# Optimization experiments

Measured on AMD Instinct MI355X. Metric: run time of the kernel, lower is better.

## Reference

```python
import jax, jax.numpy as jnp
import numpy as np

B, S, H = 4, 1024, 2560          # batch, seq, hidden_size
E, K, F = 32, 6, 1536            # num_experts, top_k, moe_intermediate_size
SHARED_F = 2 * 1536              # moe_num_shared_experts * moe_intermediate_size
NORM_MIN = 1e-12                 # config.moe_norm_min


def setup_inputs() -> dict:
    key = jax.random.key(0)
    ks = jax.random.split(key, 9)
    rnd = lambda k, shape, scale=0.02: jax.random.normal(k, shape, dtype=jnp.float32) * scale
    return {
        "hidden_states": jax.random.normal(ks[0], (B, S, H), dtype=jnp.float32),
        "router_w": rnd(ks[1], (E, H)),              # Ernie4_5_MoeTopKRouter.weight (fp32)
        "router_bias": jnp.zeros((E,), jnp.float32),  # moe_statics.e_score_correction_bias
        "gate_w": rnd(ks[2], (E, H, F)),
        "up_w": rnd(ks[3], (E, H, F)),
        "down_w": rnd(ks[4], (E, F, H)),
        "shared_gate_w": rnd(ks[5], (H, SHARED_F)),
        "shared_up_w": rnd(ks[6], (H, SHARED_F)),
        "shared_down_w": rnd(ks[7], (SHARED_F, H)),
    }


def _mlp(x, gw, uw, dw):
    # Ernie4_5_MoeMLP: down( silu(gate(x)) * up(x) ), no biases
    return (jax.nn.silu(x @ gw) * (x @ uw)) @ dw


def _forward(hidden_states, router_w, router_bias, gate_w, up_w, down_w,
             shared_gate_w, shared_up_w, shared_down_w):
    T = B * S
    xt = hidden_states.reshape(T, H)

    # shared experts path (always-on dense MLP)
    shared_out = _mlp(xt, shared_gate_w, shared_up_w, shared_down_w)

    # router: fp32 linear -> softmax -> (+ correction bias) -> top-k -> renorm
    logits = xt.astype(jnp.float32) @ router_w.T            # [T, E]
    probs = jax.nn.softmax(logits, axis=-1)
    top_w, top_i = jax.lax.top_k(probs + router_bias[None, :], K)  # [T, K]
    top_w = top_w / jnp.clip(jnp.sum(top_w, axis=-1, keepdims=True), NORM_MIN)
    top_w = top_w.astype(hidden_states.dtype)

    # expert combine: loop over the fixed expert set; per-token combine weight
    # cw[t] = sum_k top_w[t,k] * (top_i[t,k] == e)  (matches one-hot dispatch +
    # index_add_ scatter combine of the original)
    out = jnp.zeros_like(xt)
    for e in range(E):
        cw = jnp.sum(jnp.where(top_i == e, top_w, 0.0), axis=-1)  # [T]
        y = _mlp(xt, gate_w[e], up_w[e], down_w[e])               # [T, H]
        out = out + cw[:, None] * y

    out = out + shared_out
    return out.reshape(B, S, H)


def reference(hidden_states, router_w, router_bias, gate_w, up_w, down_w,
              shared_gate_w, shared_up_w, shared_down_w):
    return _forward(hidden_states, router_w, router_bias, gate_w, up_w, down_w,
                    shared_gate_w, shared_up_w, shared_down_w)
```

## Files before the change

kernel.cpp:

```cpp
#include <hip/hip_runtime.h>
#include <hip/hip_bf16.h>
#include <math.h>

#define T_TOK 4096
#define HID   2560
#define NEXP  32
#define KTOP  6
#define FF    1536
#define SFF   3072
#define MAXP  (T_TOK*KTOP)

typedef __attribute__((ext_vector_type(8))) short short8;
typedef __attribute__((ext_vector_type(4))) float f32x4;

static __device__ __forceinline__ unsigned short f2bf(float x){
  return __builtin_bit_cast(unsigned short, (__bf16)x);
}
static __device__ __forceinline__ float bf2f(unsigned short u){
  unsigned int x = ((unsigned int)u) << 16;
  return __builtin_bit_cast(float, x);
}

static __device__ __forceinline__ void gload_lds16(const void* g, void* l){
  __builtin_amdgcn_global_load_lds(
      (const __attribute__((address_space(1))) unsigned int*)g,
      (__attribute__((address_space(3))) unsigned int*)l, 16, 0, 0);
}

__global__ void k_cast_x(const float* __restrict__ x, unsigned short* __restrict__ xb){
  int i = (blockIdx.x * 256 + threadIdx.x) * 4;
  float4 v = *(const float4*)(x + i);
  ushort4 o;
  o.x = f2bf(v.x); o.y = f2bf(v.y); o.z = f2bf(v.z); o.w = f2bf(v.w);
  *(ushort4*)(xb + i) = o;
}

__global__ __launch_bounds__(256)
void k_transpose(const float* __restrict__ in, unsigned short* __restrict__ out,
                 const int R, const int C, const long long outBS){
  const size_t bi = (size_t)blockIdx.z * (size_t)R * C;
  const size_t bo = (size_t)blockIdx.z * (size_t)outBS;
  __shared__ unsigned short t2[64][72];
  const int r0 = blockIdx.y * 64, c0 = blockIdx.x * 64;
  const int tid = threadIdx.x;
  const int cr = tid & 15;
  const int rr = tid >> 4;
#pragma unroll
  for (int i = 0; i < 4; ++i){
    const int r = rr + 16*i;
    float4 v = *(const float4*)(in + bi + (size_t)(r0 + r)*C + c0 + cr*4);
    ushort4 p;
    p.x = f2bf(v.x); p.y = f2bf(v.y); p.z = f2bf(v.z); p.w = f2bf(v.w);
    *(ushort4*)(&t2[r][cr*4]) = p;
  }
  __syncthreads();
  const int rw = tid & 7;
  const int ro = tid >> 3;
#pragma unroll
  for (int i = 0; i < 2; ++i){
    const int c = ro + 32*i;
    ushort4 a, b;
    a.x = t2[rw*8+0][c]; a.y = t2[rw*8+1][c]; a.z = t2[rw*8+2][c]; a.w = t2[rw*8+3][c];
    b.x = t2[rw*8+4][c]; b.y = t2[rw*8+5][c]; b.z = t2[rw*8+6][c]; b.w = t2[rw*8+7][c];
    unsigned short* op = out + bo + (size_t)(c0 + c)*R + r0 + rw*8;
    *(ushort4*)(op)     = a;
    *(ushort4*)(op + 4) = b;
  }
}

__global__ void k_router(const float* __restrict__ x, const float* __restrict__ rw,
                         const float* __restrict__ rb, float* __restrict__ top_w,
                         int* __restrict__ top_i, int* __restrict__ counts){
  const int lane = threadIdx.x & 63;
  const int wv   = threadIdx.x >> 6;
  const int t    = blockIdx.x * 4 + wv;
  const float* xr = x + (size_t)t * HID;
  float xv[40];
#pragma unroll
  for (int i = 0; i < 40; ++i) xv[i] = xr[lane + 64*i];
  float sc[32];
  for (int e = 0; e < 32; ++e){
    const float* w = rw + (size_t)e * HID;
    float s = 0.f;
#pragma unroll
    for (int i = 0; i < 40; ++i) s = fmaf(xv[i], w[lane + 64*i], s);
#pragma unroll
    for (int o = 32; o; o >>= 1) s += __shfl_xor(s, o);
    sc[e] = s;
  }
  float mx = sc[0];
#pragma unroll
  for (int e = 1; e < 32; ++e) mx = fmaxf(mx, sc[e]);
  float se = 0.f;
#pragma unroll
  for (int e = 0; e < 32; ++e){ sc[e] = expf(sc[e] - mx); se += sc[e]; }
  const float inv = 1.f / se;
#pragma unroll
  for (int e = 0; e < 32; ++e) sc[e] = sc[e] * inv + rb[e];

  unsigned chosen = 0; float swv[KTOP]; int sid[KTOP]; float wsum = 0.f;
#pragma unroll
  for (int k = 0; k < KTOP; ++k){
    float bv = -1e30f; int bi = 0;
#pragma unroll
    for (int e = 0; e < 32; ++e){
      bool ok = !((chosen >> e) & 1u);
      if (ok && sc[e] > bv){ bv = sc[e]; bi = e; }
    }
    chosen |= 1u << bi; swv[k] = bv; sid[k] = bi; wsum += bv;
  }
  const float dn = fmaxf(wsum, 1e-12f);
  if (lane < KTOP){
    top_w[t*KTOP + lane] = swv[lane] / dn;
    top_i[t*KTOP + lane] = sid[lane];
    atomicAdd(counts + sid[lane], 1);
  }
}

__global__ void k_scan(const int* __restrict__ counts, int* __restrict__ offsets){
  if (threadIdx.x == 0){
    int a = 0;
    for (int e = 0; e < NEXP; ++e){ offsets[e] = a; a += counts[e]; }
    offsets[NEXP] = a;
  }
}

__global__ void k_scatter(const int* __restrict__ top_i, const float* __restrict__ top_w,
                          const int* __restrict__ offsets, int* __restrict__ cursor,
                          int* __restrict__ pair_tok, float* __restrict__ pair_w){
  const int t = blockIdx.x * 256 + threadIdx.x;
  if (t >= T_TOK) return;
#pragma unroll
  for (int k = 0; k < KTOP; ++k){
    int e = top_i[t*KTOP + k];
    int pos = offsets[e] + atomicAdd(cursor + e, 1);
    pair_tok[pos] = t;
    pair_w[pos]   = top_w[t*KTOP + k];
  }
}

template<int F8>
__global__ __launch_bounds__(256)
void k_swiglu(const unsigned short* __restrict__ y, unsigned short* __restrict__ act){
  const int i = blockIdx.x * 256 + threadIdx.x;
  const int p = i / F8, c = i % F8;
  const unsigned short* row = y + (size_t)p * (2*F8*8);
  short8 g8 = *(const short8*)(row + c*8);
  short8 u8 = *(const short8*)(row + F8*8 + c*8);
  short8 o;
#pragma unroll
  for (int j = 0; j < 8; ++j){
    float g = bf2f((unsigned short)g8[j]);
    float u = bf2f((unsigned short)u8[j]);
    float s = (g / (1.f + expf(-g))) * u;
    o[j] = (short)f2bf(s);
  }
  *(short8*)(act + (size_t)p*F8*8 + c*8) = o;
}

template<bool GROUPED, bool GATHER, int OUT>
__global__ __launch_bounds__(512, 2)
void k_gemm(const unsigned short* __restrict__ A,
            const unsigned short* __restrict__ BT,
            void* __restrict__ outp,
            const int* __restrict__ pair_tok, const float* __restrict__ pair_w,
            const int* __restrict__ counts, const int* __restrict__ offsets,
            const int N, const int K, const int ntiles)
{
  const int NH = K >> 5;
  const int total = gridDim.x;
  const int phys  = blockIdx.x;
  const int logical = (phys & 7) * (total >> 3) + (phys >> 3);
  const int mt   = logical & 15;
  const int rest = logical >> 4;
  const int n0 = (rest % ntiles) << 8;
  const int e  = rest / ntiles;

  int M, base;
  if (GROUPED){ M = counts[e]; base = offsets[e]; }
  else        { M = T_TOK;     base = 0; }
  if (mt * 256 >= M) return;
  const unsigned short* Bb = BT + (size_t)e * (size_t)N * K;

  __shared__ unsigned short AS[4*8192];
  __shared__ unsigned short BS[4*8192];

  const int tid  = threadIdx.x;
  const int lane = tid & 63;
  const int w    = tid >> 6;
  const int wr = w >> 2, wc = w & 3;

  const int lrow = lane >> 2, lchunk = lane & 3;
  const int swz = (lchunk ^ ((lrow >> 1) & 3)) * 8;
  const unsigned short *ap0, *ap1, *bp0, *bp1;
  {
    const int r0 = w*32 + lrow, r1 = w*32 + 16 + lrow;
    int i0 = min(mt*256 + r0, M - 1);
    int i1 = min(mt*256 + r1, M - 1);
    int rowA0 = GATHER ? pair_tok[base + i0] : (GROUPED ? base + i0 : i0);
    int rowA1 = GATHER ? pair_tok[base + i1] : (GROUPED ? base + i1 : i1);
    ap0 = A + (size_t)rowA0 * K + swz;
    ap1 = A + (size_t)rowA1 * K + swz;
    bp0 = Bb + (size_t)(n0 + r0) * K + swz;
    bp1 = Bb + (size_t)(n0 + r1) * K + swz;
  }

  const f32x4 zero = {0.f,0.f,0.f,0.f};
  f32x4 acc[8][4];
#pragma unroll
  for (int m = 0; m < 8; ++m)
#pragma unroll
    for (int n = 0; n < 4; ++n) acc[m][n] = zero;

  const int fr = lane & 15;
  const int fg = ((lane >> 4) ^ ((lane >> 1) & 3)) * 16;

#define STAGE(h)                                                            \
  { const int _s = (h) & 3; const size_t _k = (size_t)(h) * 32;             \
    gload_lds16(ap0 + _k, (char*)AS + _s*16384 + (w*32)*64);                \
    gload_lds16(ap1 + _k, (char*)AS + _s*16384 + (w*32+16)*64);             \
    gload_lds16(bp0 + _k, (char*)BS + _s*16384 + (w*32)*64);                \
    gload_lds16(bp1 + _k, (char*)BS + _s*16384 + (w*32+16)*64); }

  STAGE(0) STAGE(1) STAGE(2)
  asm volatile("s_waitcnt vmcnt(8)" ::: "memory");
  __builtin_amdgcn_s_barrier();

#pragma unroll 4
  for (int h = 0; h < NH; ++h){
    const int s = h & 3;
    const char* _as = (const char*)AS + s*16384;
    const char* _bs = (const char*)BS + s*16384;
    short8 bq[4], af[8];
#pragma unroll
    for (int n = 0; n < 4; ++n)
      bq[n] = *(const short8*)(_bs + (wc*64 + n*16 + fr)*64 + fg);
#pragma unroll
    for (int m = 0; m < 8; ++m)
      af[m] = *(const short8*)(_as + (wr*128 + m*16 + fr)*64 + fg);
    if (h + 3 < NH) STAGE(h + 3)
    __builtin_amdgcn_s_setprio(1);
#pragma unroll
    for (int m = 0; m < 8; ++m)
#pragma unroll
      for (int n = 0; n < 4; ++n)
        acc[m][n] = __builtin_amdgcn_mfma_f32_16x16x32_bf16(af[m], bq[n], acc[m][n], 0, 0, 0);
    __builtin_amdgcn_s_setprio(0);
    if (h + 3 < NH)      asm volatile("s_waitcnt vmcnt(8)" ::: "memory");
    else if (h + 2 < NH) asm volatile("s_waitcnt vmcnt(4)" ::: "memory");
    else if (h + 1 < NH) asm volatile("s_waitcnt vmcnt(0)" ::: "memory");
    __builtin_amdgcn_s_barrier();
  }
#undef STAGE

#pragma unroll
  for (int m = 0; m < 8; ++m)
#pragma unroll
    for (int j = 0; j < 4; ++j){
      const int rr = mt*256 + wr*128 + m*16 + (lane >> 4)*4 + j;
      if (rr < M){
        const int col = n0 + wc*64 + (lane & 15);
        if (OUT == 0){
          unsigned short* orow = (unsigned short*)outp + (size_t)(base + rr) * N + col;
#pragma unroll
          for (int n = 0; n < 4; ++n) orow[n*16] = f2bf(acc[m][n][j]);
        } else if (OUT == 1){
          const int p = base + rr;
          const int tok = pair_tok[p];
          const float pw = pair_w[p];
          float* orow = (float*)outp + (size_t)tok * HID + col;
#pragma unroll
          for (int n = 0; n < 4; ++n) atomicAdd(orow + n*16, acc[m][n][j] * pw);
        } else {
          float* orow = (float*)outp + (size_t)rr * N + col;
#pragma unroll
          for (int n = 0; n < 4; ++n) orow[n*16] = acc[m][n][j];
        }
      }
    }
}

extern "C" void kernel_launch(void* const* d_in, const int* in_sizes, int n_in,
                              void* d_out, int out_size, void* d_ws, size_t ws_size,
                              hipStream_t stream)
{
  (void)in_sizes; (void)n_in; (void)out_size; (void)ws_size;
  const float* hid = (const float*)d_in[0];
  const float* rw  = (const float*)d_in[1];
  const float* rb  = (const float*)d_in[2];
  const float* gw  = (const float*)d_in[3];
  const float* uw  = (const float*)d_in[4];
  const float* dw  = (const float*)d_in[5];
  const float* sgw = (const float*)d_in[6];
  const float* suw = (const float*)d_in[7];
  const float* sdw = (const float*)d_in[8];
  float* out = (float*)d_out;

  char* ws = (char*)d_ws;
  size_t o = 0;
  unsigned short* xb   = (unsigned short*)(ws + o); o += (size_t)T_TOK*HID*2;
  unsigned short* act  = (unsigned short*)(ws + o); o += (size_t)MAXP*FF*2;
  unsigned short* sact = (unsigned short*)(ws + o); o += (size_t)T_TOK*SFF*2;
  unsigned short* y    = (unsigned short*)(ws + o); o += (size_t)MAXP*2*FF*2;
  unsigned short* sy   = (unsigned short*)(ws + o); o += (size_t)T_TOK*2*SFF*2;
  unsigned short* Wbuf = (unsigned short*)(ws + o);
  unsigned short* guT  = Wbuf;
  unsigned short* sguT = Wbuf + (size_t)NEXP*2*FF*HID;
  unsigned short* dT   = Wbuf;
  unsigned short* sdT  = Wbuf + (size_t)NEXP*HID*FF;
  o += (size_t)NEXP*2*FF*HID*2 + (size_t)2*SFF*HID*2;
  float* top_w    = (float*)(ws + o); o += (size_t)T_TOK*KTOP*4;
  int*   top_i    = (int*)(ws + o);   o += (size_t)T_TOK*KTOP*4;
  float* pair_w   = (float*)(ws + o); o += (size_t)MAXP*4;
  int*   pair_tok = (int*)(ws + o);   o += (size_t)MAXP*4;
  int*   counts   = (int*)(ws + o);   o += NEXP*4;
  int*   offsets  = (int*)(ws + o);   o += (NEXP+1)*4;
  int*   cursor   = (int*)(ws + o);   o += NEXP*4;

  hipMemsetAsync(counts, 0, (NEXP + (NEXP+1) + NEXP) * sizeof(int), stream);

  k_cast_x<<<(T_TOK*HID)/1024, 256, 0, stream>>>(hid, xb);
  k_router<<<T_TOK/4, 256, 0, stream>>>(hid, rw, rb, top_w, top_i, counts);
  k_scan<<<1, 64, 0, stream>>>(counts, offsets);
  k_scatter<<<T_TOK/256, 256, 0, stream>>>(top_i, top_w, offsets, cursor, pair_tok, pair_w);

  k_transpose<<<dim3(FF/64,  HID/64, NEXP), 256, 0, stream>>>(gw,  guT,                    HID, FF,  (long long)2*FF*HID);
  k_transpose<<<dim3(FF/64,  HID/64, NEXP), 256, 0, stream>>>(uw,  guT + (size_t)FF*HID,   HID, FF,  (long long)2*FF*HID);
  k_transpose<<<dim3(SFF/64, HID/64, 1),    256, 0, stream>>>(sgw, sguT,                   HID, SFF, 0);
  k_transpose<<<dim3(SFF/64, HID/64, 1),    256, 0, stream>>>(suw, sguT + (size_t)SFF*HID, HID, SFF, 0);

  k_gemm<true,  true,  0><<<16*(2*FF/256)*NEXP, 512, 0, stream>>>(
      xb, guT, y, pair_tok, nullptr, counts, offsets, 2*FF, HID, 2*FF/256);
  k_gemm<false, false, 0><<<16*(2*SFF/256), 512, 0, stream>>>(
      xb, sguT, sy, nullptr, nullptr, nullptr, nullptr, 2*SFF, HID, 2*SFF/256);
  k_swiglu<FF/8><<<(MAXP*(FF/8))/256, 256, 0, stream>>>(y, act);
  k_swiglu<SFF/8><<<(T_TOK*(SFF/8))/256, 256, 0, stream>>>(sy, sact);

  k_transpose<<<dim3(HID/64, FF/64,  NEXP), 256, 0, stream>>>(dw,  dT,  FF,  HID, (long long)HID*FF);
  k_transpose<<<dim3(HID/64, SFF/64, 1),    256, 0, stream>>>(sdw, sdT, SFF, HID, 0);

  k_gemm<false, false, 2><<<16*(HID/256), 512, 0, stream>>>(
      sact, sdT, out, nullptr, nullptr, nullptr, nullptr, HID, SFF, HID/256);
  k_gemm<true,  false, 1><<<16*(HID/256)*NEXP, 512, 0, stream>>>(
      act, dT, out, pair_tok, pair_w, counts, offsets, HID, FF, HID/256);
}
```

Measured before the change: 1.792 ms.

## Fuse SwiGLU into gate/up GEMM epilogue and merge expert/shared launches

Replaces the separate gate/up GEMMs and SwiGLU kernels with one kernel that computes gate and up accumulators side by side over 128-wide column tiles and applies silu(g)*u in the epilogue, writing bf16 activations directly. Expert and shared tiles are merged into a single grid. This removes the large intermediate y/sy round-trip through memory and several launches. Both GEMM loops now prefetch LDS fragments for the next step after the MFMAs, behind a sched_barrier, and use a shallower vmcnt wait. The cost is a narrower N tile with two accumulator sets, which changes register pressure and A-tile reuse per block.

```diff
diff --git a/kernel.cpp b/kernel.cpp
--- a/kernel.cpp
+++ b/kernel.cpp
@@ -15,10 +15,6 @@
 
 static __device__ __forceinline__ unsigned short f2bf(float x){
   return __builtin_bit_cast(unsigned short, (__bf16)x);
-}
-static __device__ __forceinline__ float bf2f(unsigned short u){
-  unsigned int x = ((unsigned int)u) << 16;
-  return __builtin_bit_cast(float, x);
 }
 
 static __device__ __forceinline__ void gload_lds16(const void* g, void* l){
@@ -139,34 +135,148 @@
   }
 }
 
-template<int F8>
-__global__ __launch_bounds__(256)
-void k_swiglu(const unsigned short* __restrict__ y, unsigned short* __restrict__ act){
-  const int i = blockIdx.x * 256 + threadIdx.x;
-  const int p = i / F8, c = i % F8;
-  const unsigned short* row = y + (size_t)p * (2*F8*8);
-  short8 g8 = *(const short8*)(row + c*8);
-  short8 u8 = *(const short8*)(row + F8*8 + c*8);
-  short8 o;
-#pragma unroll
-  for (int j = 0; j < 8; ++j){
-    float g = bf2f((unsigned short)g8[j]);
-    float u = bf2f((unsigned short)u8[j]);
-    float s = (g / (1.f + expf(-g))) * u;
-    o[j] = (short)f2bf(s);
-  }
-  *(short8*)(act + (size_t)p*F8*8 + c*8) = o;
-}
-
-template<bool GROUPED, bool GATHER, int OUT>
 __global__ __launch_bounds__(512, 2)
-void k_gemm(const unsigned short* __restrict__ A,
-            const unsigned short* __restrict__ BT,
-            void* __restrict__ outp,
+void k_gufused(const unsigned short* __restrict__ A,
+               const unsigned short* __restrict__ gT, const unsigned short* __restrict__ uT,
+               const unsigned short* __restrict__ sgT, const unsigned short* __restrict__ suT,
+               unsigned short* __restrict__ act, unsigned short* __restrict__ sact,
+               const int* __restrict__ pair_tok,
+               const int* __restrict__ counts, const int* __restrict__ offsets)
+{
+  constexpr int K = HID;
+  constexpr int NH = K >> 5;
+  constexpr int EXPTILES = NEXP * (FF/128);
+  const int total = gridDim.x;
+  const int phys  = blockIdx.x;
+  const int logical = (phys & 7) * (total >> 3) + (phys >> 3);
+  const int mt   = logical & 15;
+  const int rest = logical >> 4;
+
+  int M, base, n0, N; bool gather;
+  const unsigned short *Bg, *Bu; unsigned short* op;
+  if (rest < EXPTILES){
+    const int e = rest / (FF/128);
+    n0 = (rest % (FF/128)) * 128;
+    M = counts[e]; base = offsets[e]; gather = true;
+    Bg = gT + (size_t)e * FF * HID; Bu = uT + (size_t)e * FF * HID;
+    op = act; N = FF;
+  } else {
+    const int s = rest - EXPTILES;
+    n0 = s * 128; M = T_TOK; base = 0; gather = false;
+    Bg = sgT; Bu = suT; op = sact; N = SFF;
+  }
+  if (mt * 256 >= M) return;
+
+  __shared__ unsigned short AS[4*8192];
+  __shared__ unsigned short BgS[4*4096];
+  __shared__ unsigned short BuS[4*4096];
+
+  const int tid  = threadIdx.x;
+  const int lane = tid & 63;
+  const int w    = tid >> 6;
+  const int wr = w >> 1, wc = w & 1;
+
+  const int lrow = lane >> 2, lchunk = lane & 3;
+  const int swz = (lchunk ^ ((lrow >> 1) & 3)) * 8;
+  const unsigned short *ap0, *ap1, *bgp, *bup;
+  {
+    const int r0 = w*32 + lrow, r1 = w*32 + 16 + lrow;
+    int i0 = min(mt*256 + r0, M - 1);
+    int i1 = min(mt*256 + r1, M - 1);
+    int rowA0 = gather ? pair_tok[base + i0] : i0;
+    int rowA1 = gather ? pair_tok[base + i1] : i1;
+    ap0 = A + (size_t)rowA0 * K + swz;
+    ap1 = A + (size_t)rowA1 * K + swz;
+    const int rb = w*16 + lrow;
+    const int swzb = (lchunk ^ ((rb >> 1) & 3)) * 8;
+    bgp = Bg + (size_t)(n0 + rb) * K + swzb;
+    bup = Bu + (size_t)(n0 + rb) * K + swzb;
+  }
+
+  const f32x4 zero = {0.f,0.f,0.f,0.f};
+  f32x4 accg[4][4], accu[4][4];
+#pragma unroll
+  for (int m = 0; m < 4; ++m)
+#pragma unroll
+    for (int n = 0; n < 4; ++n){ accg[m][n] = zero; accu[m][n] = zero; }
+
+  const int fr = lane & 15;
+  const int fg = ((lane >> 4) ^ ((lane >> 1) & 3)) * 16;
+  short8 af[4], bg[4], bu[4];
+
+#define GU_STAGE(h)                                                         \
+  { const int _s = (h) & 3; const size_t _k = (size_t)(h) * 32;             \
+    gload_lds16(ap0 + _k, (char*)AS  + _s*16384 + (w*32)*64);               \
+    gload_lds16(ap1 + _k, (char*)AS  + _s*16384 + (w*32+16)*64);            \
+    gload_lds16(bgp + _k, (char*)BgS + _s*8192  + (w*16)*64);               \
+    gload_lds16(bup + _k, (char*)BuS + _s*8192  + (w*16)*64); }
+
+#define GU_RFRAGS(h)                                                        \
+  { const int _s = (h) & 3;                                                 \
+    const char* _as = (const char*)AS  + _s*16384;                          \
+    const char* _bg = (const char*)BgS + _s*8192;                           \
+    const char* _bu = (const char*)BuS + _s*8192;                           \
+    _Pragma("unroll")                                                       \
+    for (int m = 0; m < 4; ++m)                                             \
+      af[m] = *(const short8*)(_as + (wr*64 + m*16 + fr)*64 + fg);          \
+    _Pragma("unroll")                                                       \
+    for (int n = 0; n < 4; ++n){                                            \
+      bg[n] = *(const short8*)(_bg + (wc*64 + n*16 + fr)*64 + fg);          \
+      bu[n] = *(const short8*)(_bu + (wc*64 + n*16 + fr)*64 + fg); } }
+
+  GU_STAGE(0) GU_STAGE(1) GU_STAGE(2)
+  asm volatile("s_waitcnt vmcnt(4)" ::: "memory");
+  __builtin_amdgcn_s_barrier();
+  GU_RFRAGS(0)
+
+#pragma unroll 4
+  for (int h = 0; h < NH; ++h){
+    __builtin_amdgcn_s_setprio(1);
+#pragma unroll
+    for (int m = 0; m < 4; ++m)
+#pragma unroll
+      for (int n = 0; n < 4; ++n){
+        accg[m][n] = __builtin_amdgcn_mfma_f32_16x16x32_bf16(af[m], bg[n], accg[m][n], 0, 0, 0);
+        accu[m][n] = __builtin_amdgcn_mfma_f32_16x16x32_bf16(af[m], bu[n], accu[m][n], 0, 0, 0);
+      }
+    __builtin_amdgcn_s_setprio(0);
+    __builtin_amdgcn_sched_barrier(0);
+    if (h + 3 < NH) GU_STAGE(h + 3)
+    if (h + 1 < NH) GU_RFRAGS(h + 1)
+    if (h + 3 < NH) asm volatile("s_waitcnt vmcnt(4)" ::: "memory");
+    else            asm volatile("s_waitcnt vmcnt(0)" ::: "memory");
+    __builtin_amdgcn_s_barrier();
+  }
+#undef GU_STAGE
+#undef GU_RFRAGS
+
+#pragma unroll
+  for (int m = 0; m < 4; ++m)
+#pragma unroll
+    for (int j = 0; j < 4; ++j){
+      const int rr = mt*256 + wr*64 + m*16 + (lane >> 4)*4 + j;
+      if (rr < M){
+        unsigned short* orow = op + (size_t)(base + rr) * N + n0 + wc*64 + fr;
+#pragma unroll
+        for (int n = 0; n < 4; ++n){
+          float g = accg[m][n][j], u = accu[m][n][j];
+          float s = (g / (1.f + expf(-g))) * u;
+          orow[n*16] = f2bf(s);
+        }
+      }
+    }
+}
+
+template<bool GROUPED, int OUT>
+__global__ __launch_bounds__(512, 2)
+void k_down(const unsigned short* __restrict__ Aact,
+            const unsigned short* __restrict__ BT, float* __restrict__ outp,
             const int* __restrict__ pair_tok, const float* __restrict__ pair_w,
             const int* __restrict__ counts, const int* __restrict__ offsets,
-            const int N, const int K, const int ntiles)
+            const int K)
 {
+  constexpr int N = HID;
+  constexpr int ntiles = N >> 8;
   const int NH = K >> 5;
   const int total = gridDim.x;
   const int phys  = blockIdx.x;
@@ -197,10 +307,8 @@
     const int r0 = w*32 + lrow, r1 = w*32 + 16 + lrow;
     int i0 = min(mt*256 + r0, M - 1);
     int i1 = min(mt*256 + r1, M - 1);
-    int rowA0 = GATHER ? pair_tok[base + i0] : (GROUPED ? base + i0 : i0);
-    int rowA1 = GATHER ? pair_tok[base + i1] : (GROUPED ? base + i1 : i1);
-    ap0 = A + (size_t)rowA0 * K + swz;
-    ap1 = A + (size_t)rowA1 * K + swz;
+    ap0 = Aact + (size_t)(base + i0) * K + swz;
+    ap1 = Aact + (size_t)(base + i1) * K + swz;
     bp0 = Bb + (size_t)(n0 + r0) * K + swz;
     bp1 = Bb + (size_t)(n0 + r1) * K + swz;
   }
@@ -214,31 +322,33 @@
 
   const int fr = lane & 15;
   const int fg = ((lane >> 4) ^ ((lane >> 1) & 3)) * 16;
-
-#define STAGE(h)                                                            \
+  short8 af[8], bq[4];
+
+#define DN_STAGE(h)                                                         \
   { const int _s = (h) & 3; const size_t _k = (size_t)(h) * 32;             \
     gload_lds16(ap0 + _k, (char*)AS + _s*16384 + (w*32)*64);                \
     gload_lds16(ap1 + _k, (char*)AS + _s*16384 + (w*32+16)*64);             \
     gload_lds16(bp0 + _k, (char*)BS + _s*16384 + (w*32)*64);                \
     gload_lds16(bp1 + _k, (char*)BS + _s*16384 + (w*32+16)*64); }
 
-  STAGE(0) STAGE(1) STAGE(2)
-  asm volatile("s_waitcnt vmcnt(8)" ::: "memory");
+#define DN_RFRAGS(h)                                                        \
+  { const int _s = (h) & 3;                                                 \
+    const char* _as = (const char*)AS + _s*16384;                           \
+    const char* _bs = (const char*)BS + _s*16384;                           \
+    _Pragma("unroll")                                                       \
+    for (int m = 0; m < 8; ++m)                                             \
+      af[m] = *(const short8*)(_as + (wr*128 + m*16 + fr)*64 + fg);         \
+    _Pragma("unroll")                                                       \
+    for (int n = 0; n < 4; ++n)                                             \
+      bq[n] = *(const short8*)(_bs + (wc*64 + n*16 + fr)*64 + fg); }
+
+  DN_STAGE(0) DN_STAGE(1) DN_STAGE(2)
+  asm volatile("s_waitcnt vmcnt(4)" ::: "memory");
   __builtin_amdgcn_s_barrier();
+  DN_RFRAGS(0)
 
 #pragma unroll 4
   for (int h = 0; h < NH; ++h){
-    const int s = h & 3;
-    const char* _as = (const char*)AS + s*16384;
-    const char* _bs = (const char*)BS + s*16384;
-    short8 bq[4], af[8];
-#pragma unroll
-    for (int n = 0; n < 4; ++n)
-      bq[n] = *(const short8*)(_bs + (wc*64 + n*16 + fr)*64 + fg);
-#pragma unroll
-    for (int m = 0; m < 8; ++m)
-      af[m] = *(const short8*)(_as + (wr*128 + m*16 + fr)*64 + fg);
-    if (h + 3 < NH) STAGE(h + 3)
     __builtin_amdgcn_s_setprio(1);
 #pragma unroll
     for (int m = 0; m < 8; ++m)
@@ -246,12 +356,15 @@
       for (int n = 0; n < 4; ++n)
         acc[m][n] = __builtin_amdgcn_mfma_f32_16x16x32_bf16(af[m], bq[n], acc[m][n], 0, 0, 0);
     __builtin_amdgcn_s_setprio(0);
-    if (h + 3 < NH)      asm volatile("s_waitcnt vmcnt(8)" ::: "memory");
-    else if (h + 2 < NH) asm volatile("s_waitcnt vmcnt(4)" ::: "memory");
-    else if (h + 1 < NH) asm volatile("s_waitcnt vmcnt(0)" ::: "memory");
+    __builtin_amdgcn_sched_barrier(0);
+    if (h + 3 < NH) DN_STAGE(h + 3)
+    if (h + 1 < NH) DN_RFRAGS(h + 1)
+    if (h + 3 < NH) asm volatile("s_waitcnt vmcnt(4)" ::: "memory");
+    else            asm volatile("s_waitcnt vmcnt(0)" ::: "memory");
     __builtin_amdgcn_s_barrier();
   }
-#undef STAGE
+#undef DN_STAGE
+#undef DN_RFRAGS
 
 #pragma unroll
   for (int m = 0; m < 8; ++m)
@@ -259,20 +372,16 @@
     for (int j = 0; j < 4; ++j){
       const int rr = mt*256 + wr*128 + m*16 + (lane >> 4)*4 + j;
       if (rr < M){
-        const int col = n0 + wc*64 + (lane & 15);
-        if (OUT == 0){
-          unsigned short* orow = (unsigned short*)outp + (size_t)(base + rr) * N + col;
-#pragma unroll
-          for (int n = 0; n < 4; ++n) orow[n*16] = f2bf(acc[m][n][j]);
-        } else if (OUT == 1){
+        const int col = n0 + wc*64 + fr;
+        if (OUT == 1){
           const int p = base + rr;
           const int tok = pair_tok[p];
           const float pw = pair_w[p];
-          float* orow = (float*)outp + (size_t)tok * HID + col;
+          float* orow = outp + (size_t)tok * HID + col;
 #pragma unroll
           for (int n = 0; n < 4; ++n) atomicAdd(orow + n*16, acc[m][n][j] * pw);
         } else {
-          float* orow = (float*)outp + (size_t)rr * N + col;
+          float* orow = outp + (size_t)rr * N + col;
 #pragma unroll
           for (int n = 0; n < 4; ++n) orow[n*16] = acc[m][n][j];
         }
@@ -301,14 +410,14 @@
   unsigned short* xb   = (unsigned short*)(ws + o); o += (size_t)T_TOK*HID*2;
   unsigned short* act  = (unsigned short*)(ws + o); o += (size_t)MAXP*FF*2;
   unsigned short* sact = (unsigned short*)(ws + o); o += (size_t)T_TOK*SFF*2;
-  unsigned short* y    = (unsigned short*)(ws + o); o += (size_t)MAXP*2*FF*2;
-  unsigned short* sy   = (unsigned short*)(ws + o); o += (size_t)T_TOK*2*SFF*2;
   unsigned short* Wbuf = (unsigned short*)(ws + o);
-  unsigned short* guT  = Wbuf;
-  unsigned short* sguT = Wbuf + (size_t)NEXP*2*FF*HID;
-  unsigned short* dT   = Wbuf;
-  unsigned short* sdT  = Wbuf + (size_t)NEXP*HID*FF;
-  o += (size_t)NEXP*2*FF*HID*2 + (size_t)2*SFF*HID*2;
+  unsigned short* gT  = Wbuf;
+  unsigned short* uT  = Wbuf + (size_t)NEXP*FF*HID;
+  unsigned short* sgT = Wbuf + (size_t)2*NEXP*FF*HID;
+  unsigned short* suT = sgT + (size_t)SFF*HID;
+  unsigned short* dT  = Wbuf;
+  unsigned short* sdT = Wbuf + (size_t)NEXP*FF*HID;
+  o += (size_t)2*NEXP*FF*HID*2 + (size_t)2*SFF*HID*2;
   float* top_w    = (float*)(ws + o); o += (size_t)T_TOK*KTOP*4;
   int*   top_i    = (int*)(ws + o);   o += (size_t)T_TOK*KTOP*4;
   float* pair_w   = (float*)(ws + o); o += (size_t)MAXP*4;
@@ -324,23 +433,19 @@
   k_scan<<<1, 64, 0, stream>>>(counts, offsets);
   k_scatter<<<T_TOK/256, 256, 0, stream>>>(top_i, top_w, offsets, cursor, pair_tok, pair_w);
 
-  k_transpose<<<dim3(FF/64,  HID/64, NEXP), 256, 0, stream>>>(gw,  guT,                    HID, FF,  (long long)2*FF*HID);
-  k_transpose<<<dim3(FF/64,  HID/64, NEXP), 256, 0, stream>>>(uw,  guT + (size_t)FF*HID,   HID, FF,  (long long)2*FF*HID);
-  k_transpose<<<dim3(SFF/64, HID/64, 1),    256, 0, stream>>>(sgw, sguT,                   HID, SFF, 0);
-  k_transpose<<<dim3(SFF/64, HID/64, 1),    256, 0, stream>>>(suw, sguT + (size_t)SFF*HID, HID, SFF, 0);
-
-  k_gemm<true,  true,  0><<<16*(2*FF/256)*NEXP, 512, 0, stream>>>(
-      xb, guT, y, pair_tok, nullptr, counts, offsets, 2*FF, HID, 2*FF/256);
-  k_gemm<false, false, 0><<<16*(2*SFF/256), 512, 0, stream>>>(
-      xb, sguT, sy, nullptr, nullptr, nullptr, nullptr, 2*SFF, HID, 2*SFF/256);
-  k_swiglu<FF/8><<<(MAXP*(FF/8))/256, 256, 0, stream>>>(y, act);
-  k_swiglu<SFF/8><<<(T_TOK*(SFF/8))/256, 256, 0, stream>>>(sy, sact);
+  k_transpose<<<dim3(FF/64,  HID/64, NEXP), 256, 0, stream>>>(gw,  gT,  HID, FF,  (long long)FF*HID);
+  k_transpose<<<dim3(FF/64,  HID/64, NEXP), 256, 0, stream>>>(uw,  uT,  HID, FF,  (long long)FF*HID);
+  k_transpose<<<dim3(SFF/64, HID/64, 1),    256, 0, stream>>>(sgw, sgT, HID, SFF, 0);
+  k_transpose<<<dim3(SFF/64, HID/64, 1),    256, 0, stream>>>(suw, suT, HID, SFF, 0);
+
+  k_gufused<<<16*(NEXP*(FF/128) + SFF/128), 512, 0, stream>>>(
+      xb, gT, uT, sgT, suT, act, sact, pair_tok, counts, offsets);
 
   k_transpose<<<dim3(HID/64, FF/64,  NEXP), 256, 0, stream>>>(dw,  dT,  FF,  HID, (long long)HID*FF);
   k_transpose<<<dim3(HID/64, SFF/64, 1),    256, 0, stream>>>(sdw, sdT, SFF, HID, 0);
 
-  k_gemm<false, false, 2><<<16*(HID/256), 512, 0, stream>>>(
-      sact, sdT, out, nullptr, nullptr, nullptr, nullptr, HID, SFF, HID/256);
-  k_gemm<true,  false, 1><<<16*(HID/256)*NEXP, 512, 0, stream>>>(
-      act, dT, out, pair_tok, pair_w, counts, offsets, HID, FF, HID/256);
-}
+  k_down<false, 2><<<16*(HID/256), 512, 0, stream>>>(
+      sact, sdT, out, nullptr, nullptr, nullptr, nullptr, SFF);
+  k_down<true, 1><<<16*(HID/256)*NEXP, 512, 0, stream>>>(
+      act, dT, out, pair_tok, pair_w, counts, offsets, FF);
+}
```

New measurement: 3.437 ms. 91.8% more time.

## Fuse SwiGLU into gate/up GEMM epilogue and merge shared/routed expert launches

Applied to the files above, without the earlier changes.

Gate and up weight columns are interleaved during the transpose so each lane pair holds matching gate/up outputs. The SwiGLU is then computed in the GEMM epilogue with a lane shuffle, which removes the intermediate y/sy buffers and the separate swiglu kernels. Routed and shared experts are merged into single launches for both the gate/up and down GEMMs. The shared down projection now accumulates atomically into a zeroed output, which needs an extra memset and adds atomic traffic in exchange for fewer launches and better load balance.

```diff
diff --git a/kernel.cpp b/kernel.cpp
--- a/kernel.cpp
+++ b/kernel.cpp
@@ -16,10 +16,6 @@
 static __device__ __forceinline__ unsigned short f2bf(float x){
   return __builtin_bit_cast(unsigned short, (__bf16)x);
 }
-static __device__ __forceinline__ float bf2f(unsigned short u){
-  unsigned int x = ((unsigned int)u) << 16;
-  return __builtin_bit_cast(float, x);
-}
 
 static __device__ __forceinline__ void gload_lds16(const void* g, void* l){
   __builtin_amdgcn_global_load_lds(
@@ -37,7 +33,8 @@
 
 __global__ __launch_bounds__(256)
 void k_transpose(const float* __restrict__ in, unsigned short* __restrict__ out,
-                 const int R, const int C, const long long outBS){
+                 const int R, const int C, const long long outBS,
+                 const int colmul, const int coladd){
   const size_t bi = (size_t)blockIdx.z * (size_t)R * C;
   const size_t bo = (size_t)blockIdx.z * (size_t)outBS;
   __shared__ unsigned short t2[64][72];
@@ -62,7 +59,7 @@
     ushort4 a, b;
     a.x = t2[rw*8+0][c]; a.y = t2[rw*8+1][c]; a.z = t2[rw*8+2][c]; a.w = t2[rw*8+3][c];
     b.x = t2[rw*8+4][c]; b.y = t2[rw*8+5][c]; b.z = t2[rw*8+6][c]; b.w = t2[rw*8+7][c];
-    unsigned short* op = out + bo + (size_t)(c0 + c)*R + r0 + rw*8;
+    unsigned short* op = out + bo + (size_t)(colmul*(c0 + c) + coladd)*R + r0 + rw*8;
     *(ushort4*)(op)     = a;
     *(ushort4*)(op + 4) = b;
   }
@@ -139,48 +136,35 @@
   }
 }
 
-template<int F8>
-__global__ __launch_bounds__(256)
-void k_swiglu(const unsigned short* __restrict__ y, unsigned short* __restrict__ act){
-  const int i = blockIdx.x * 256 + threadIdx.x;
-  const int p = i / F8, c = i % F8;
-  const unsigned short* row = y + (size_t)p * (2*F8*8);
-  short8 g8 = *(const short8*)(row + c*8);
-  short8 u8 = *(const short8*)(row + F8*8 + c*8);
-  short8 o;
-#pragma unroll
-  for (int j = 0; j < 8; ++j){
-    float g = bf2f((unsigned short)g8[j]);
-    float u = bf2f((unsigned short)u8[j]);
-    float s = (g / (1.f + expf(-g))) * u;
-    o[j] = (short)f2bf(s);
-  }
-  *(short8*)(act + (size_t)p*F8*8 + c*8) = o;
-}
-
-template<bool GROUPED, bool GATHER, int OUT>
 __global__ __launch_bounds__(512, 2)
-void k_gemm(const unsigned short* __restrict__ A,
-            const unsigned short* __restrict__ BT,
-            void* __restrict__ outp,
-            const int* __restrict__ pair_tok, const float* __restrict__ pair_w,
-            const int* __restrict__ counts, const int* __restrict__ offsets,
-            const int N, const int K, const int ntiles)
+void k_gu(const unsigned short* __restrict__ A,
+          const unsigned short* __restrict__ guT, const unsigned short* __restrict__ sguT,
+          unsigned short* __restrict__ act, unsigned short* __restrict__ sact,
+          const int* __restrict__ pair_tok,
+          const int* __restrict__ counts, const int* __restrict__ offsets)
 {
-  const int NH = K >> 5;
+  constexpr int K = HID;
+  constexpr int NH = K >> 5;
+  constexpr int EXPT = NEXP * (2*FF/256);
   const int total = gridDim.x;
   const int phys  = blockIdx.x;
   const int logical = (phys & 7) * (total >> 3) + (phys >> 3);
   const int mt   = logical & 15;
   const int rest = logical >> 4;
-  const int n0 = (rest % ntiles) << 8;
-  const int e  = rest / ntiles;
-
-  int M, base;
-  if (GROUPED){ M = counts[e]; base = offsets[e]; }
-  else        { M = T_TOK;     base = 0; }
+
+  int M, base, n0, Fout; bool gather;
+  const unsigned short* Bb; unsigned short* op;
+  if (rest < EXPT){
+    const int e = rest / 12;
+    n0 = (rest % 12) << 8;
+    M = counts[e]; base = offsets[e]; gather = true;
+    Bb = guT + (size_t)e * (2*FF) * HID; op = act; Fout = FF;
+  } else {
+    const int s = rest - EXPT;
+    n0 = s << 8; M = T_TOK; base = 0; gather = false;
+    Bb = sguT; op = sact; Fout = SFF;
+  }
   if (mt * 256 >= M) return;
-  const unsigned short* Bb = BT + (size_t)e * (size_t)N * K;
 
   __shared__ unsigned short AS[4*8192];
   __shared__ unsigned short BS[4*8192];
@@ -197,8 +181,8 @@
     const int r0 = w*32 + lrow, r1 = w*32 + 16 + lrow;
     int i0 = min(mt*256 + r0, M - 1);
     int i1 = min(mt*256 + r1, M - 1);
-    int rowA0 = GATHER ? pair_tok[base + i0] : (GROUPED ? base + i0 : i0);
-    int rowA1 = GATHER ? pair_tok[base + i1] : (GROUPED ? base + i1 : i1);
+    int rowA0 = gather ? pair_tok[base + i0] : i0;
+    int rowA1 = gather ? pair_tok[base + i1] : i1;
     ap0 = A + (size_t)rowA0 * K + swz;
     ap1 = A + (size_t)rowA1 * K + swz;
     bp0 = Bb + (size_t)(n0 + r0) * K + swz;
@@ -253,29 +237,136 @@
   }
 #undef STAGE
 
+  const int fb = (n0 >> 1) + wc*32 + (fr >> 1);
 #pragma unroll
   for (int m = 0; m < 8; ++m)
 #pragma unroll
     for (int j = 0; j < 4; ++j){
       const int rr = mt*256 + wr*128 + m*16 + (lane >> 4)*4 + j;
       if (rr < M){
-        const int col = n0 + wc*64 + (lane & 15);
-        if (OUT == 0){
-          unsigned short* orow = (unsigned short*)outp + (size_t)(base + rr) * N + col;
-#pragma unroll
-          for (int n = 0; n < 4; ++n) orow[n*16] = f2bf(acc[m][n][j]);
-        } else if (OUT == 1){
-          const int p = base + rr;
-          const int tok = pair_tok[p];
-          const float pw = pair_w[p];
-          float* orow = (float*)outp + (size_t)tok * HID + col;
-#pragma unroll
-          for (int n = 0; n < 4; ++n) atomicAdd(orow + n*16, acc[m][n][j] * pw);
-        } else {
-          float* orow = (float*)outp + (size_t)rr * N + col;
-#pragma unroll
-          for (int n = 0; n < 4; ++n) orow[n*16] = acc[m][n][j];
+        unsigned short* orow = op + (size_t)(base + rr) * Fout + fb;
+#pragma unroll
+        for (int n = 0; n < 4; ++n){
+          float g = acc[m][n][j];
+          float u = __shfl_xor(g, 1);
+          float sv = (g / (1.f + expf(-g))) * u;
+          if (!(lane & 1)) orow[n*8] = f2bf(sv);
         }
+      }
+    }
+}
+
+__global__ __launch_bounds__(512, 2)
+void k_dn(const unsigned short* __restrict__ act, const unsigned short* __restrict__ sact,
+          const unsigned short* __restrict__ dT, const unsigned short* __restrict__ sdT,
+          float* __restrict__ outp,
+          const int* __restrict__ pair_tok, const float* __restrict__ pair_w,
+          const int* __restrict__ counts, const int* __restrict__ offsets)
+{
+  constexpr int EXPT = NEXP * (HID/256);
+  const int total = gridDim.x;
+  const int phys  = blockIdx.x;
+  const int logical = (phys & 7) * (total >> 3) + (phys >> 3);
+  const int mt   = logical & 15;
+  const int rest = logical >> 4;
+
+  int M, base, n0, K; bool grouped;
+  const unsigned short *Aarr, *Bb;
+  if (rest < EXPT){
+    const int e = rest / (HID/256);
+    n0 = (rest % (HID/256)) << 8;
+    M = counts[e]; base = offsets[e]; grouped = true;
+    Aarr = act; K = FF; Bb = dT + (size_t)e * HID * FF;
+  } else {
+    const int s = rest - EXPT;
+    n0 = s << 8; M = T_TOK; base = 0; grouped = false;
+    Aarr = sact; K = SFF; Bb = sdT;
+  }
+  if (mt * 256 >= M) return;
+  const int NH = K >> 5;
+
+  __shared__ unsigned short AS[4*8192];
+  __shared__ unsigned short BS[4*8192];
+
+  const int tid  = threadIdx.x;
+  const int lane = tid & 63;
+  const int w    = tid >> 6;
+  const int wr = w >> 2, wc = w & 3;
+
+  const int lrow = lane >> 2, lchunk = lane & 3;
+  const int swz = (lchunk ^ ((lrow >> 1) & 3)) * 8;
+  const unsigned short *ap0, *ap1, *bp0, *bp1;
+  {
+    const int r0 = w*32 + lrow, r1 = w*32 + 16 + lrow;
+    int i0 = min(mt*256 + r0, M - 1);
+    int i1 = min(mt*256 + r1, M - 1);
+    ap0 = Aarr + (size_t)(base + i0) * K + swz;
+    ap1 = Aarr + (size_t)(base + i1) * K + swz;
+    bp0 = Bb + (size_t)(n0 + r0) * K + swz;
+    bp1 = Bb + (size_t)(n0 + r1) * K + swz;
+  }
+
+  const f32x4 zero = {0.f,0.f,0.f,0.f};
+  f32x4 acc[8][4];
+#pragma unroll
+  for (int m = 0; m < 8; ++m)
+#pragma unroll
+    for (int n = 0; n < 4; ++n) acc[m][n] = zero;
+
+  const int fr = lane & 15;
+  const int fg = ((lane >> 4) ^ ((lane >> 1) & 3)) * 16;
+
+#define STAGE(h)                                                            \
+  { const int _s = (h) & 3; const size_t _k = (size_t)(h) * 32;             \
+    gload_lds16(ap0 + _k, (char*)AS + _s*16384 + (w*32)*64);                \
+    gload_lds16(ap1 + _k, (char*)AS + _s*16384 + (w*32+16)*64);             \
+    gload_lds16(bp0 + _k, (char*)BS + _s*16384 + (w*32)*64);                \
+    gload_lds16(bp1 + _k, (char*)BS + _s*16384 + (w*32+16)*64); }
+
+  STAGE(0) STAGE(1) STAGE(2)
+  asm volatile("s_waitcnt vmcnt(8)" ::: "memory");
+  __builtin_amdgcn_s_barrier();
+
+#pragma unroll 4
+  for (int h = 0; h < NH; ++h){
+    const int s = h & 3;
+    const char* _as = (const char*)AS + s*16384;
+    const char* _bs = (const char*)BS + s*16384;
+    short8 bq[4], af[8];
+#pragma unroll
+    for (int n = 0; n < 4; ++n)
+      bq[n] = *(const short8*)(_bs + (wc*64 + n*16 + fr)*64 + fg);
+#pragma unroll
+    for (int m = 0; m < 8; ++m)
+      af[m] = *(const short8*)(_as + (wr*128 + m*16 + fr)*64 + fg);
+    if (h + 3 < NH) STAGE(h + 3)
+    __builtin_amdgcn_s_setprio(1);
+#pragma unroll
+    for (int m = 0; m < 8; ++m)
+#pragma unroll
+      for (int n = 0; n < 4; ++n)
+        acc[m][n] = __builtin_amdgcn_mfma_f32_16x16x32_bf16(af[m], bq[n], acc[m][n], 0, 0, 0);
+    __builtin_amdgcn_s_setprio(0);
+    if (h + 3 < NH)      asm volatile("s_waitcnt vmcnt(8)" ::: "memory");
+    else if (h + 2 < NH) asm volatile("s_waitcnt vmcnt(4)" ::: "memory");
+    else if (h + 1 < NH) asm volatile("s_waitcnt vmcnt(0)" ::: "memory");
+    __builtin_amdgcn_s_barrier();
+  }
+#undef STAGE
+
+#pragma unroll
+  for (int m = 0; m < 8; ++m)
+#pragma unroll
+    for (int j = 0; j < 4; ++j){
+      const int rr = mt*256 + wr*128 + m*16 + (lane >> 4)*4 + j;
+      if (rr < M){
+        const int col = n0 + wc*64 + fr;
+        int tok; float pw;
+        if (grouped){ tok = pair_tok[base + rr]; pw = pair_w[base + rr]; }
+        else        { tok = rr; pw = 1.f; }
+        float* orow = outp + (size_t)tok * HID + col;
+#pragma unroll
+        for (int n = 0; n < 4; ++n) atomicAdd(orow + n*16, acc[m][n][j] * pw);
       }
     }
 }
@@ -301,8 +392,6 @@
   unsigned short* xb   = (unsigned short*)(ws + o); o += (size_t)T_TOK*HID*2;
   unsigned short* act  = (unsigned short*)(ws + o); o += (size_t)MAXP*FF*2;
   unsigned short* sact = (unsigned short*)(ws + o); o += (size_t)T_TOK*SFF*2;
-  unsigned short* y    = (unsigned short*)(ws + o); o += (size_t)MAXP*2*FF*2;
-  unsigned short* sy   = (unsigned short*)(ws + o); o += (size_t)T_TOK*2*SFF*2;
   unsigned short* Wbuf = (unsigned short*)(ws + o);
   unsigned short* guT  = Wbuf;
   unsigned short* sguT = Wbuf + (size_t)NEXP*2*FF*HID;
@@ -318,29 +407,24 @@
   int*   cursor   = (int*)(ws + o);   o += NEXP*4;
 
   hipMemsetAsync(counts, 0, (NEXP + (NEXP+1) + NEXP) * sizeof(int), stream);
+  hipMemsetAsync(out, 0, (size_t)T_TOK*HID*sizeof(float), stream);
 
   k_cast_x<<<(T_TOK*HID)/1024, 256, 0, stream>>>(hid, xb);
   k_router<<<T_TOK/4, 256, 0, stream>>>(hid, rw, rb, top_w, top_i, counts);
   k_scan<<<1, 64, 0, stream>>>(counts, offsets);
   k_scatter<<<T_TOK/256, 256, 0, stream>>>(top_i, top_w, offsets, cursor, pair_tok, pair_w);
 
-  k_transpose<<<dim3(FF/64,  HID/64, NEXP), 256, 0, stream>>>(gw,  guT,                    HID, FF,  (long long)2*FF*HID);
-  k_transpose<<<dim3(FF/64,  HID/64, NEXP), 256, 0, stream>>>(uw,  guT + (size_t)FF*HID,   HID, FF,  (long long)2*FF*HID);
-  k_transpose<<<dim3(SFF/64, HID/64, 1),    256, 0, stream>>>(sgw, sguT,                   HID, SFF, 0);
-  k_transpose<<<dim3(SFF/64, HID/64, 1),    256, 0, stream>>>(suw, sguT + (size_t)SFF*HID, HID, SFF, 0);
-
-  k_gemm<true,  true,  0><<<16*(2*FF/256)*NEXP, 512, 0, stream>>>(
-      xb, guT, y, pair_tok, nullptr, counts, offsets, 2*FF, HID, 2*FF/256);
-  k_gemm<false, false, 0><<<16*(2*SFF/256), 512, 0, stream>>>(
-      xb, sguT, sy, nullptr, nullptr, nullptr, nullptr, 2*SFF, HID, 2*SFF/256);
-  k_swiglu<FF/8><<<(MAXP*(FF/8))/256, 256, 0, stream>>>(y, act);
-  k_swiglu<SFF/8><<<(T_TOK*(SFF/8))/256, 256, 0, stream>>>(sy, sact);
-
-  k_transpose<<<dim3(HID/64, FF/64,  NEXP), 256, 0, stream>>>(dw,  dT,  FF,  HID, (long long)HID*FF);
-  k_transpose<<<dim3(HID/64, SFF/64, 1),    256, 0, stream>>>(sdw, sdT, SFF, HID, 0);
-
-  k_gemm<false, false, 2><<<16*(HID/256), 512, 0, stream>>>(
-      sact, sdT, out, nullptr, nullptr, nullptr, nullptr, HID, SFF, HID/256);
-  k_gemm<true,  false, 1><<<16*(HID/256)*NEXP, 512, 0, stream>>>(
-      act, dT, out, pair_tok, pair_w, counts, offsets, HID, FF, HID/256);
-}
+  k_transpose<<<dim3(FF/64,  HID/64, NEXP), 256, 0, stream>>>(gw,  guT,  HID, FF,  (long long)2*FF*HID, 2, 0);
+  k_transpose<<<dim3(FF/64,  HID/64, NEXP), 256, 0, stream>>>(uw,  guT,  HID, FF,  (long long)2*FF*HID, 2, 1);
+  k_transpose<<<dim3(SFF/64, HID/64, 1),    256, 0, stream>>>(sgw, sguT, HID, SFF, 0, 2, 0);
+  k_transpose<<<dim3(SFF/64, HID/64, 1),    256, 0, stream>>>(suw, sguT, HID, SFF, 0, 2, 1);
+
+  k_gu<<<16*(NEXP*(2*FF/256) + 2*SFF/256), 512, 0, stream>>>(
+      xb, guT, sguT, act, sact, pair_tok, counts, offsets);
+
+  k_transpose<<<dim3(HID/64, FF/64,  NEXP), 256, 0, stream>>>(dw,  dT,  FF,  HID, (long long)HID*FF, 1, 0);
+  k_transpose<<<dim3(HID/64, SFF/64, 1),    256, 0, stream>>>(sdw, sdT, SFF, HID, 0, 1, 0);
+
+  k_dn<<<16*(NEXP*(HID/256) + HID/256), 512, 0, stream>>>(
+      act, sact, dT, sdT, out, pair_tok, pair_w, counts, offsets);
+}
```

Result: slower. 2.796 ms (+56.0%).

## Fuse SwiGLU activation into gate/up GEMM epilogue with paired gate and up tiles

Applied to the files above, without the earlier changes.

Adds a dedicated gate/up GEMM kernel that computes matching gate and up column tiles together (128 columns each) and applies silu(g)*u in the epilogue. It writes the bf16 activation directly and drops the separate swiglu kernels and the intermediate y/sy buffers. This removes a full write and re-read of the 2F-wide intermediate for both routed and shared experts. The tile per block changes from 256x256 to 256x128x2 with 4x4 accumulators per operand, which alters register pressure and the LDS layout.

```diff
diff --git a/kernel.cpp b/kernel.cpp
--- a/kernel.cpp
+++ b/kernel.cpp
@@ -15,10 +15,6 @@
 
 static __device__ __forceinline__ unsigned short f2bf(float x){
   return __builtin_bit_cast(unsigned short, (__bf16)x);
-}
-static __device__ __forceinline__ float bf2f(unsigned short u){
-  unsigned int x = ((unsigned int)u) << 16;
-  return __builtin_bit_cast(float, x);
 }
 
 static __device__ __forceinline__ void gload_lds16(const void* g, void* l){
@@ -139,23 +135,126 @@
   }
 }
 
-template<int F8>
-__global__ __launch_bounds__(256)
-void k_swiglu(const unsigned short* __restrict__ y, unsigned short* __restrict__ act){
-  const int i = blockIdx.x * 256 + threadIdx.x;
-  const int p = i / F8, c = i % F8;
-  const unsigned short* row = y + (size_t)p * (2*F8*8);
-  short8 g8 = *(const short8*)(row + c*8);
-  short8 u8 = *(const short8*)(row + F8*8 + c*8);
-  short8 o;
-#pragma unroll
-  for (int j = 0; j < 8; ++j){
-    float g = bf2f((unsigned short)g8[j]);
-    float u = bf2f((unsigned short)u8[j]);
-    float s = (g / (1.f + expf(-g))) * u;
-    o[j] = (short)f2bf(s);
-  }
-  *(short8*)(act + (size_t)p*F8*8 + c*8) = o;
+template<bool EXP>
+__global__ __launch_bounds__(512, 2)
+void k_gufuse(const unsigned short* __restrict__ A,
+              const unsigned short* __restrict__ guT,
+              unsigned short* __restrict__ op,
+              const int* __restrict__ pair_tok,
+              const int* __restrict__ counts, const int* __restrict__ offsets,
+              const int Fout)
+{
+  constexpr int K = HID;
+  constexpr int NH = K >> 5;
+  const int ntiles = Fout >> 7;
+  const int total = gridDim.x;
+  const int phys  = blockIdx.x;
+  const int logical = (phys & 7) * (total >> 3) + (phys >> 3);
+  const int mt   = logical & 15;
+  const int rest = logical >> 4;
+  const int n0 = (rest % ntiles) << 7;
+  const int e  = rest / ntiles;
+
+  int M, base;
+  if (EXP){ M = counts[e]; base = offsets[e]; }
+  else    { M = T_TOK;     base = 0; }
+  if (mt * 256 >= M) return;
+  const unsigned short* Bb = guT + (size_t)e * (size_t)(2*Fout) * K;
+
+  __shared__ unsigned short AS[4*8192];
+  __shared__ unsigned short BgS[4*4096];
+  __shared__ unsigned short BuS[4*4096];
+
+  const int tid  = threadIdx.x;
+  const int lane = tid & 63;
+  const int w    = tid >> 6;
+  const int wr = w >> 1, wc = w & 1;
+
+  const int lrow = lane >> 2, lchunk = lane & 3;
+  const unsigned short *ap0, *ap1, *bgp, *bup;
+  {
+    const int r0 = w*32 + lrow, r1 = w*32 + 16 + lrow;
+    const int swza = (lchunk ^ ((r0 >> 1) & 3)) * 8;
+    int i0 = min(mt*256 + r0, M - 1);
+    int i1 = min(mt*256 + r1, M - 1);
+    int rowA0 = EXP ? pair_tok[base + i0] : i0;
+    int rowA1 = EXP ? pair_tok[base + i1] : i1;
+    ap0 = A + (size_t)rowA0 * K + swza;
+    ap1 = A + (size_t)rowA1 * K + swza;
+    const int rb = w*16 + lrow;
+    const int swzb = (lchunk ^ ((rb >> 1) & 3)) * 8;
+    bgp = Bb + (size_t)(n0 + rb) * K + swzb;
+    bup = Bb + (size_t)(Fout + n0 + rb) * K + swzb;
+  }
+
+  const f32x4 zero = {0.f,0.f,0.f,0.f};
+  f32x4 accg[4][4], accu[4][4];
+#pragma unroll
+  for (int m = 0; m < 4; ++m)
+#pragma unroll
+    for (int n = 0; n < 4; ++n){ accg[m][n] = zero; accu[m][n] = zero; }
+
+  const int fr = lane & 15;
+  const int fg = ((lane >> 4) ^ ((lane >> 1) & 3)) * 16;
+
+#define STAGE(h)                                                            \
+  { const int _s = (h) & 3; const size_t _k = (size_t)(h) * 32;             \
+    gload_lds16(ap0 + _k, (char*)AS  + _s*16384 + (w*32)*64);               \
+    gload_lds16(ap1 + _k, (char*)AS  + _s*16384 + (w*32+16)*64);            \
+    gload_lds16(bgp + _k, (char*)BgS + _s*8192  + (w*16)*64);               \
+    gload_lds16(bup + _k, (char*)BuS + _s*8192  + (w*16)*64); }
+
+  STAGE(0) STAGE(1) STAGE(2)
+  asm volatile("s_waitcnt vmcnt(8)" ::: "memory");
+  __builtin_amdgcn_s_barrier();
+
+#pragma unroll 4
+  for (int h = 0; h < NH; ++h){
+    const int s = h & 3;
+    const char* _as = (const char*)AS  + s*16384;
+    const char* _bg = (const char*)BgS + s*8192;
+    const char* _bu = (const char*)BuS + s*8192;
+    short8 af[4], bg[4], bu[4];
+#pragma unroll
+    for (int n = 0; n < 4; ++n){
+      bg[n] = *(const short8*)(_bg + (wc*64 + n*16 + fr)*64 + fg);
+      bu[n] = *(const short8*)(_bu + (wc*64 + n*16 + fr)*64 + fg);
+    }
+#pragma unroll
+    for (int m = 0; m < 4; ++m)
+      af[m] = *(const short8*)(_as + (wr*64 + m*16 + fr)*64 + fg);
+    if (h + 3 < NH) STAGE(h + 3)
+    __builtin_amdgcn_s_setprio(1);
+#pragma unroll
+    for (int m = 0; m < 4; ++m)
+#pragma unroll
+      for (int n = 0; n < 4; ++n){
+        accg[m][n] = __builtin_amdgcn_mfma_f32_16x16x32_bf16(af[m], bg[n], accg[m][n], 0, 0, 0);
+        accu[m][n] = __builtin_amdgcn_mfma_f32_16x16x32_bf16(af[m], bu[n], accu[m][n], 0, 0, 0);
+      }
+    __builtin_amdgcn_s_setprio(0);
+    if (h + 3 < NH)      asm volatile("s_waitcnt vmcnt(8)" ::: "memory");
+    else if (h + 2 < NH) asm volatile("s_waitcnt vmcnt(4)" ::: "memory");
+    else if (h + 1 < NH) asm volatile("s_waitcnt vmcnt(0)" ::: "memory");
+    __builtin_amdgcn_s_barrier();
+  }
+#undef STAGE
+
+#pragma unroll
+  for (int m = 0; m < 4; ++m)
+#pragma unroll
+    for (int j = 0; j < 4; ++j){
+      const int rr = mt*256 + wr*64 + m*16 + (lane >> 4)*4 + j;
+      if (rr < M){
+        unsigned short* orow = op + (size_t)(base + rr) * Fout + n0 + wc*64 + fr;
+#pragma unroll
+        for (int n = 0; n < 4; ++n){
+          float g = accg[m][n][j], u = accu[m][n][j];
+          float sv = (g / (1.f + expf(-g))) * u;
+          orow[n*16] = f2bf(sv);
+        }
+      }
+    }
 }
 
 template<bool GROUPED, bool GATHER, int OUT>
@@ -259,12 +358,8 @@
     for (int j = 0; j < 4; ++j){
       const int rr = mt*256 + wr*128 + m*16 + (lane >> 4)*4 + j;
       if (rr < M){
-        const int col = n0 + wc*64 + (lane & 15);
-        if (OUT == 0){
-          unsigned short* orow = (unsigned short*)outp + (size_t)(base + rr) * N + col;
-#pragma unroll
-          for (int n = 0; n < 4; ++n) orow[n*16] = f2bf(acc[m][n][j]);
-        } else if (OUT == 1){
+        const int col = n0 + wc*64 + fr;
+        if (OUT == 1){
           const int p = base + rr;
           const int tok = pair_tok[p];
           const float pw = pair_w[p];
@@ -301,8 +396,6 @@
   unsigned short* xb   = (unsigned short*)(ws + o); o += (size_t)T_TOK*HID*2;
   unsigned short* act  = (unsigned short*)(ws + o); o += (size_t)MAXP*FF*2;
   unsigned short* sact = (unsigned short*)(ws + o); o += (size_t)T_TOK*SFF*2;
-  unsigned short* y    = (unsigned short*)(ws + o); o += (size_t)MAXP*2*FF*2;
-  unsigned short* sy   = (unsigned short*)(ws + o); o += (size_t)T_TOK*2*SFF*2;
   unsigned short* Wbuf = (unsigned short*)(ws + o);
   unsigned short* guT  = Wbuf;
   unsigned short* sguT = Wbuf + (size_t)NEXP*2*FF*HID;
@@ -329,12 +422,10 @@
   k_transpose<<<dim3(SFF/64, HID/64, 1),    256, 0, stream>>>(sgw, sguT,                   HID, SFF, 0);
   k_transpose<<<dim3(SFF/64, HID/64, 1),    256, 0, stream>>>(suw, sguT + (size_t)SFF*HID, HID, SFF, 0);
 
-  k_gemm<true,  true,  0><<<16*(2*FF/256)*NEXP, 512, 0, stream>>>(
-      xb, guT, y, pair_tok, nullptr, counts, offsets, 2*FF, HID, 2*FF/256);
-  k_gemm<false, false, 0><<<16*(2*SFF/256), 512, 0, stream>>>(
-      xb, sguT, sy, nullptr, nullptr, nullptr, nullptr, 2*SFF, HID, 2*SFF/256);
-  k_swiglu<FF/8><<<(MAXP*(FF/8))/256, 256, 0, stream>>>(y, act);
-  k_swiglu<SFF/8><<<(T_TOK*(SFF/8))/256, 256, 0, stream>>>(sy, sact);
+  k_gufuse<true><<<16*(FF/128)*NEXP, 512, 0, stream>>>(
+      xb, guT, act, pair_tok, counts, offsets, FF);
+  k_gufuse<false><<<16*(SFF/128), 512, 0, stream>>>(
+      xb, sguT, sact, nullptr, nullptr, nullptr, SFF);
 
   k_transpose<<<dim3(HID/64, FF/64,  NEXP), 256, 0, stream>>>(dw,  dT,  FF,  HID, (long long)HID*FF);
   k_transpose<<<dim3(HID/64, SFF/64, 1),    256, 0, stream>>>(sdw, sdT, SFF, HID, 0);
```

Result: slower. 1.884 ms (+5.2%).
